# Kernel optimization log

Measured on AMD Instinct MI355X. Metric: run time of the kernel, lower is better.

## Reference

```python
import jax, jax.numpy as jnp
import numpy as np

H = 16      # num_heads
HD = 64     # head_dim
W = 1024    # local window size
G = 256     # number of global tokens
EPS = 1e-6
NEG = -1e30


def setup_inputs() -> dict:
    key = jax.random.key(0)
    ks = jax.random.split(key, 7)
    B, S, D = 1, 8192, 1024
    inner = H * HD
    s = 0.02
    return {
        "x": jax.random.normal(ks[0], (B, S, D), jnp.float32),
        "norm_w": jnp.ones((D,), jnp.float32),
        "w_q": jax.random.normal(ks[1], (D, inner), jnp.float32) * s,
        "w_k": jax.random.normal(ks[2], (D, inner), jnp.float32) * s,
        "w_v": jax.random.normal(ks[3], (D, inner), jnp.float32) * s,
        "w_out": jax.random.normal(ks[4], (inner, D), jnp.float32) * s,
        "scorer_w": jax.random.normal(ks[5], (D, 1), jnp.float32) * s,
        "scorer_b": jnp.zeros((1,), jnp.float32),
    }


def reference(x, norm_w, w_q, w_k, w_v, w_out, scorer_w, scorer_b):
    B, S, D = x.shape
    # pre-norm (RMSNorm)
    h = x * jax.lax.rsqrt(jnp.mean(x * x, axis=-1, keepdims=True) + EPS) * norm_w

    def proj(w):  # [B,S,D] -> [B,H,S,HD]
        return jnp.einsum('bsd,de->bse', h, w).reshape(B, S, H, HD).transpose(0, 2, 1, 3)

    q, k, v = proj(w_q), proj(w_k), proj(w_v)
    scale = HD ** -0.5

    # --- local block attention (non-overlapping causal windows) ---
    nW = S // W
    qw = q.reshape(B, H, nW, W, HD)
    kw = k.reshape(B, H, nW, W, HD)
    vw = v.reshape(B, H, nW, W, HD)
    ll = jnp.einsum('bhnqd,bhnkd->bhnqk', qw, kw) * scale  # [B,H,nW,W,W]
    cm = jnp.tril(jnp.ones((W, W), bool))
    ll = jnp.where(cm, ll, NEG).reshape(B, H, S, W)

    # --- sparse global attention over top-G important tokens ---
    scores = (jnp.einsum('bsd,do->bso', h, scorer_w) + scorer_b)[..., 0]  # [B,S]
    _, idx = jax.lax.top_k(scores, G)                                     # [B,G]
    kg = jnp.take_along_axis(k, idx[:, None, :, None], axis=2)            # [B,H,G,HD]
    vg = jnp.take_along_axis(v, idx[:, None, :, None], axis=2)
    lg = jnp.einsum('bhsd,bhgd->bhsg', q, kg) * scale                     # [B,H,S,G]
    pos = jnp.arange(S)
    gmask = idx[:, None, None, :] <= pos[None, None, :, None]             # causal: global pos <= query pos
    lg = jnp.where(gmask, lg, NEG)

    # --- joint softmax over local window + global tokens ---
    attn = jax.nn.softmax(jnp.concatenate([ll, lg], axis=-1), axis=-1)    # [B,H,S,W+G]
    a_loc = attn[..., :W].reshape(B, H, nW, W, W)
    o = jnp.einsum('bhnqk,bhnkd->bhnqd', a_loc, vw).reshape(B, H, S, HD)
    o = o + jnp.einsum('bhsg,bhgd->bhsd', attn[..., W:], vg)

    o = o.transpose(0, 2, 1, 3).reshape(B, S, H * HD)
    return x + jnp.einsum('bse,ed->bsd', o, w_out)  # residual
```

## Files before the change

kernel.cpp:

```cpp
#include <hip/hip_runtime.h>
#include <stdint.h>

#define S_LEN 8192
#define DIM   1024
#define NH    16
#define HD    64
#define WIN   1024
#define GTOK  256
#define QKV_STRIDE (3 * DIM)

typedef __attribute__((ext_vector_type(8))) short bf16x8;
typedef __attribute__((ext_vector_type(4))) float f32x4;
typedef __attribute__((ext_vector_type(16))) float f32x16;
typedef unsigned short u16;
typedef uint32_t u32;

__device__ __forceinline__ u16 f2bf(float f) {
  union { float f; uint32_t u; } v; v.f = f;
  uint32_t r = v.u + 0x7fffu + ((v.u >> 16) & 1u);
  return (u16)(r >> 16);
}
__device__ __forceinline__ float bf2f(u16 b) {
  union { uint32_t u; float f; } v; v.u = ((uint32_t)b) << 16;
  return v.f;
}
__device__ __forceinline__ uint32_t cvtpk(float a, float b) {
  uint32_t r;
  asm("v_cvt_pk_bf16_f32 %0, %1, %2" : "=v"(r) : "v"(a), "v"(b));
  return r;
}

__device__ __forceinline__ void gload_lds16(const void* g, void* l) {
  __builtin_amdgcn_global_load_lds((const __attribute__((address_space(1))) void*)g,
                                   (__attribute__((address_space(3))) void*)l, 16, 0, 0);
}

__global__ __launch_bounds__(256) void rmsnorm_score_kernel(
    const float* __restrict__ x, const float* __restrict__ nw,
    const float* __restrict__ sw, const float* __restrict__ sb,
    u16* __restrict__ h, float* __restrict__ scores, int* __restrict__ cnt) {
  int row = blockIdx.x, tid = threadIdx.x;
  const float4* xr = (const float4*)(x + (size_t)row * DIM);
  float4 v = xr[tid];
  float ss = v.x * v.x + v.y * v.y + v.z * v.z + v.w * v.w;
#pragma unroll
  for (int o = 32; o >= 1; o >>= 1) ss += __shfl_xor(ss, o);
  __shared__ float red[4], red2[4];
  int wv = tid >> 6;
  if ((tid & 63) == 0) red[wv] = ss;
  __syncthreads();
  ss = red[0] + red[1] + red[2] + red[3];
  float rn = rsqrtf(ss * (1.0f / DIM) + 1e-6f);
  float4 w4 = ((const float4*)nw)[tid];
  float h0 = v.x * rn * w4.x, h1 = v.y * rn * w4.y;
  float h2 = v.z * rn * w4.z, h3 = v.w * rn * w4.w;
  uint64_t pack = (uint64_t)f2bf(h0) | ((uint64_t)f2bf(h1) << 16) |
                  ((uint64_t)f2bf(h2) << 32) | ((uint64_t)f2bf(h3) << 48);
  *(uint64_t*)(h + (size_t)row * DIM + tid * 4) = pack;
  float4 s4 = ((const float4*)sw)[tid];
  float sc = h0 * s4.x + h1 * s4.y + h2 * s4.z + h3 * s4.w;
#pragma unroll
  for (int o = 32; o >= 1; o >>= 1) sc += __shfl_xor(sc, o);
  if ((tid & 63) == 0) red2[wv] = sc;
  __syncthreads();
  if (tid == 0) {
    scores[row] = red2[0] + red2[1] + red2[2] + red2[3] + sb[0];
    cnt[row] = 0;
  }
}

__global__ __launch_bounds__(256) void transpose_w_kernel(
    const float* __restrict__ wq, const float* __restrict__ wk,
    const float* __restrict__ wv, const float* __restrict__ wo,
    u16* __restrict__ wqkvT, u16* __restrict__ woutT) {
  __shared__ float tile[32][33];
  int z = blockIdx.z;
  const float* src = (z == 0) ? wq : (z == 1) ? wk : (z == 2) ? wv : wo;
  u16* dst = (z < 3) ? (wqkvT + (size_t)z * DIM * DIM) : woutT;
  int tx = threadIdx.x, ty = threadIdx.y;
  int n0 = blockIdx.x * 32, k0 = blockIdx.y * 32;
#pragma unroll
  for (int i = 0; i < 4; i++)
    tile[ty + i * 8][tx] = src[(size_t)(k0 + ty + i * 8) * DIM + n0 + tx];
  __syncthreads();
#pragma unroll
  for (int i = 0; i < 4; i++)
    dst[(size_t)(n0 + ty + i * 8) * DIM + k0 + tx] = f2bf(tile[tx][ty + i * 8]);
}

__global__ __launch_bounds__(256) void topk_count_kernel(
    const float* __restrict__ scores, int* __restrict__ cnt) {
  __shared__ float sj[1024];
  int jbase = blockIdx.y * 1024;
  for (int t = threadIdx.x; t < 1024; t += 256) sj[t] = scores[jbase + t];
  __syncthreads();
  int i = blockIdx.x * 256 + threadIdx.x;
  float my = scores[i];
  int c = 0;
  const float4* s4 = (const float4*)sj;
#pragma unroll 4
  for (int j = 0; j < 256; j++) {
    float4 v = s4[j];
    int b = jbase + j * 4;
    c += (v.x > my) || (v.x == my && (b + 0) < i);
    c += (v.y > my) || (v.y == my && (b + 1) < i);
    c += (v.z > my) || (v.z == my && (b + 2) < i);
    c += (v.w > my) || (v.w == my && (b + 3) < i);
  }
  if (c) atomicAdd(&cnt[i], c);
}

__global__ __launch_bounds__(256) void topk_scatter_kernel(
    const int* __restrict__ cnt, int* __restrict__ gidx) {
  int i = blockIdx.x * 256 + threadIdx.x;
  int c = cnt[i];
  if (c < GTOK) gidx[c] = i;
}

__global__ __launch_bounds__(128) void gather_kernel(
    const u16* __restrict__ qkv, const int* __restrict__ gidx,
    u16* __restrict__ kg, u16* __restrict__ vg) {
  int g = blockIdx.x, t = threadIdx.x;
  size_t src = (size_t)gidx[g] * QKV_STRIDE;
  *(bf16x8*)(kg + (size_t)g * DIM + t * 8) = *(const bf16x8*)(qkv + src + DIM + t * 8);
  *(bf16x8*)(vg + (size_t)g * DIM + t * 8) = *(const bf16x8*)(qkv + src + 2 * DIM + t * 8);
}

template <int RESID>
__global__ __launch_bounds__(512, 2) void gemm256_kernel(
    const u16* __restrict__ A, const u16* __restrict__ B,
    u16* __restrict__ Cb, float* __restrict__ Cf, const float* __restrict__ X,
    int M, int N, int K) {
  __shared__ __align__(16) u16 As[3][256 * 64];
  __shared__ __align__(16) u16 Bs[3][128 * 64];
  const int tid = threadIdx.x;
  const int wave = tid >> 6, lane = tid & 63;
  const int l15 = lane & 15, l4 = lane >> 4;
  const int wr = wave >> 1, wc = wave & 1;
  const int mbase = blockIdx.x * 256, nbase = blockIdx.y * 128;
  const int srow = lane >> 3, schunk = lane & 7;
  const int gcol = (schunk ^ srow) * 8;

  auto stage = [&](int tt, int b) {
    const int kt = tt << 6;
#pragma unroll
    for (int q = 0; q < 4; q++) {
      int row = wave * 32 + q * 8;
      gload_lds16(A + (size_t)(mbase + row + srow) * K + kt + gcol, &As[b][row * 64]);
    }
#pragma unroll
    for (int q = 0; q < 2; q++) {
      int row = wave * 16 + q * 8;
      gload_lds16(B + (size_t)(nbase + row + srow) * K + kt + gcol, &Bs[b][row * 64]);
    }
  };

  const int nt = K >> 6;
  f32x4 acc[4][4] = {};

  stage(0, 0);
  stage(1, 1);
  asm volatile("s_waitcnt vmcnt(6)" ::: "memory");
  __builtin_amdgcn_s_barrier();
  __builtin_amdgcn_sched_barrier(0);

  int cur = 0;
  for (int t = 0; t < nt; t++) {
    int pre = cur + 2; if (pre >= 3) pre -= 3;
    if (t + 2 < nt) stage(t + 2, pre);
    const u16* Ab = &As[cur][0];
    const u16* Bb = &Bs[cur][0];
    bf16x8 bfr[4][2], af[4][2];
#pragma unroll
    for (int nf = 0; nf < 4; nf++) {
      int row = wc * 64 + nf * 16 + l15;
#pragma unroll
      for (int kk = 0; kk < 2; kk++)
        bfr[nf][kk] = *(const bf16x8*)(Bb + row * 64 + (((kk * 4 + l4) ^ (l15 & 7)) * 8));
    }
#pragma unroll
    for (int mi = 0; mi < 4; mi++) {
      int row = wr * 64 + mi * 16 + l15;
#pragma unroll
      for (int kk = 0; kk < 2; kk++)
        af[mi][kk] = *(const bf16x8*)(Ab + row * 64 + (((kk * 4 + l4) ^ (l15 & 7)) * 8));
    }
    __builtin_amdgcn_s_setprio(1);
#pragma unroll
    for (int mi = 0; mi < 4; mi++)
#pragma unroll
      for (int nf = 0; nf < 4; nf++)
#pragma unroll
        for (int kk = 0; kk < 2; kk++)
          acc[mi][nf] = __builtin_amdgcn_mfma_f32_16x16x32_bf16(af[mi][kk], bfr[nf][kk],
                                                                acc[mi][nf], 0, 0, 0);
    __builtin_amdgcn_s_setprio(0);
    if (t + 1 < nt) {
      if (t + 2 < nt) asm volatile("s_waitcnt vmcnt(6)" ::: "memory");
      else            asm volatile("s_waitcnt vmcnt(0)" ::: "memory");
      __builtin_amdgcn_s_barrier();
      __builtin_amdgcn_sched_barrier(0);
    }
    cur = (cur + 1 == 3) ? 0 : cur + 1;
  }

#pragma unroll
  for (int mi = 0; mi < 4; mi++) {
#pragma unroll
    for (int nf = 0; nf < 4; nf++) {
#pragma unroll
      for (int r = 0; r < 4; r++) {
        int row = mbase + wr * 64 + mi * 16 + l4 * 4 + r;
        int col = nbase + wc * 64 + nf * 16 + l15;
        float v = acc[mi][nf][r];
        if (RESID) Cf[(size_t)row * N + col] = X[(size_t)row * N + col] + v;
        else       Cb[(size_t)row * N + col] = f2bf(v);
      }
    }
  }
}

__global__ __launch_bounds__(512) void attn_kernel(
    const u16* __restrict__ qkv, const u16* __restrict__ kg,
    const u16* __restrict__ vg, const int* __restrict__ gidx,
    u16* __restrict__ o) {
  __shared__ u16 kT[2][64][72];
  __shared__ u16 vT[2][64][72];
  __shared__ int gposLds[2][64];
  const int tid = threadIdx.x, wave = tid >> 6, lane = tid & 63;
  const int l31 = lane & 31, hi = lane >> 5;
  const int win = blockIdx.x >> 1, pair = blockIdx.x & 1;
  const int wbase = win * WIN;
  const int hoff = blockIdx.y * HD;

  const int skey = tid >> 3, sd8 = (tid & 7) * 8;
  const int vcol = skey ^ ((sd8 >> 4) << 4);

  bf16x8 nk, nv;
  int ng = 0;
  {
    const u16* base = qkv + (size_t)(wbase + skey) * QKV_STRIDE + hoff + sd8;
    nk = *(const bf16x8*)(base + DIM);
    nv = *(const bf16x8*)(base + 2 * DIM);
  }

  for (int sp = 0; sp < 2; sp++) {
    const int j = sp ? (3 - pair) : pair;
    const int qsbase = wbase + j * 256;
    const int nLocal = (j + 1) * 4;
    const int nTiles = nLocal + GTOK / 64;
    const int qrow = qsbase + wave * 32 + l31;
    const int qwmax = qsbase + wave * 32 + 31;

    bf16x8 qf[4];
    {
      const float SC2 = 0.125f * 1.44269504088896f;
      const u16* qptr = qkv + (size_t)qrow * QKV_STRIDE + hoff + hi * 8;
#pragma unroll
      for (int ks = 0; ks < 4; ks++) {
        bf16x8 raw = *(const bf16x8*)(qptr + ks * 16);
        bf16x8 sc;
#pragma unroll
        for (int jj = 0; jj < 8; jj++) sc[jj] = (short)f2bf(bf2f((u16)raw[jj]) * SC2);
        qf[ks] = sc;
      }
    }

    f32x16 acc0 = {}, acc1 = {};
    float mr = -3.0e38f, lr = 0.f;

    __syncthreads();

    for (int t = 0; t < nTiles; t++) {
      const int p = t & 1;
      const bool isLocal = (t < nLocal);
      const int tbase = wbase + t * 64;
      *(bf16x8*)(&kT[p][skey][sd8]) = nk;
#pragma unroll
      for (int jj = 0; jj < 8; jj++) vT[p][sd8 + jj][vcol] = (u16)nv[jj];
      if (!isLocal && tid < 64) gposLds[p][tid] = ng;
      {
        const int nt = t + 1;
        const u16 *ksrc = nullptr, *vsrc = nullptr;
        if (nt < nLocal) {
          const u16* base = qkv + (size_t)(wbase + nt * 64 + skey) * QKV_STRIDE + hoff + sd8;
          ksrc = base + DIM; vsrc = base + 2 * DIM;
        } else if (nt < nTiles) {
          size_t grow = (size_t)((nt - nLocal) * 64 + skey) * DIM + hoff + sd8;
          ksrc = kg + grow; vsrc = vg + grow;
          if (tid < 64) ng = gidx[(nt - nLocal) * 64 + tid];
        } else if (sp == 0) {
          const u16* base = qkv + (size_t)(wbase + skey) * QKV_STRIDE + hoff + sd8;
          ksrc = base + DIM; vsrc = base + 2 * DIM;
        }
        if (ksrc) { nk = *(const bf16x8*)(ksrc); nv = *(const bf16x8*)(vsrc); }
      }
      __syncthreads();

      if (isLocal && tbase > qwmax) continue;

      float sv[32];
      __builtin_amdgcn_s_setprio(1);
#pragma unroll
      for (int kb = 0; kb < 2; kb++) {
        const u16* krow = &kT[p][kb * 32 + l31][hi * 8];
        bf16x8 k0 = *(const bf16x8*)(krow);
        bf16x8 k1 = *(const bf16x8*)(krow + 16);
        bf16x8 k2 = *(const bf16x8*)(krow + 32);
        bf16x8 k3 = *(const bf16x8*)(krow + 48);
        f32x16 z = {};
        z = __builtin_amdgcn_mfma_f32_32x32x16_bf16(k0, qf[0], z, 0, 0, 0);
        z = __builtin_amdgcn_mfma_f32_32x32x16_bf16(k1, qf[1], z, 0, 0, 0);
        z = __builtin_amdgcn_mfma_f32_32x32x16_bf16(k2, qf[2], z, 0, 0, 0);
        z = __builtin_amdgcn_mfma_f32_32x32x16_bf16(k3, qf[3], z, 0, 0, 0);
#pragma unroll
        for (int r = 0; r < 16; r++) sv[kb * 16 + r] = z[r];
      }
      __builtin_amdgcn_s_setprio(0);

      if (isLocal) {
        const int lim = qrow - tbase;
        if (lim < 63) {
#pragma unroll
          for (int kb = 0; kb < 2; kb++)
#pragma unroll
            for (int r = 0; r < 16; r++) {
              int crow = kb * 32 + (r & 3) + 8 * (r >> 2) + 4 * hi;
              if (crow > lim) sv[kb * 16 + r] = -3.0e38f;
            }
        }
      } else {
#pragma unroll
        for (int kb = 0; kb < 2; kb++)
#pragma unroll
          for (int r = 0; r < 16; r++) {
            int kpos = gposLds[p][kb * 32 + (r & 3) + 8 * (r >> 2) + 4 * hi];
            if (kpos > qrow) sv[kb * 16 + r] = -3.0e38f;
          }
      }

      float m0 = sv[0], m1 = sv[1], m2 = sv[2], m3 = sv[3];
#pragma unroll
      for (int i = 4; i < 32; i += 4) {
        m0 = fmaxf(m0, sv[i]);     m1 = fmaxf(m1, sv[i + 1]);
        m2 = fmaxf(m2, sv[i + 2]); m3 = fmaxf(m3, sv[i + 3]);
      }
      float vmax = fmaxf(fmaxf(m0, m1), fmaxf(m2, m3));
      vmax = fmaxf(vmax, __shfl_xor(vmax, 32));
      if (__any(vmax > mr + 11.0f)) {
        float mn = fmaxf(mr, vmax);
        float al = exp2f(mr - mn);
        lr *= al;
        mr = mn;
#pragma unroll
        for (int i = 0; i < 16; i++) { acc0[i] *= al; acc1[i] *= al; }
      }
      float s0 = 0.f, s1 = 0.f, s2 = 0.f, s3 = 0.f;
#pragma unroll
      for (int i = 0; i < 32; i += 4) {
        float p0 = exp2f(sv[i] - mr),     p1 = exp2f(sv[i + 1] - mr);
        float p2 = exp2f(sv[i + 2] - mr), p3 = exp2f(sv[i + 3] - mr);
        sv[i] = p0; sv[i + 1] = p1; sv[i + 2] = p2; sv[i + 3] = p3;
        s0 += p0; s1 += p1; s2 += p2; s3 += p3;
      }
      float ps = (s0 + s1) + (s2 + s3);
      ps += __shfl_xor(ps, 32);
      lr += ps;

      bf16x8 pf[4];
#pragma unroll
      for (int q4 = 0; q4 < 4; q4++) {
        int b = q4 * 8;
        uint32_t w0 = cvtpk(sv[b + 0], sv[b + 1]);
        uint32_t w1 = cvtpk(sv[b + 2], sv[b + 3]);
        uint32_t w2 = cvtpk(sv[b + 4], sv[b + 5]);
        uint32_t w3 = cvtpk(sv[b + 6], sv[b + 7]);
        uint32_t w0s = __shfl_xor((int)w0, 32), w2s = __shfl_xor((int)w2, 32);
        uint32_t w1s = __shfl_xor((int)w1, 32), w3s = __shfl_xor((int)w3, 32);
        union { uint32_t w[4]; bf16x8 v; } u;
        u.w[0] = hi ? w2s : w0;
        u.w[1] = hi ? w3s : w1;
        u.w[2] = hi ? w2 : w0s;
        u.w[3] = hi ? w3 : w1s;
        pf[q4] = u.v;
      }

      __builtin_amdgcn_s_setprio(1);
#pragma unroll
      for (int dblk = 0; dblk < 2; dblk++) {
        const int swz = (dblk * 2 + (l31 >> 4)) << 4;
        const u16* vrow = &vT[p][dblk * 32 + l31][0];
        f32x16 a = dblk ? acc1 : acc0;
#pragma unroll
        for (int ksg = 0; ksg < 4; ksg++) {
          bf16x8 vf = *(const bf16x8*)(vrow + ((ksg * 16 + hi * 8) ^ swz));
          a = __builtin_amdgcn_mfma_f32_32x32x16_bf16(vf, pf[ksg], a, 0, 0, 0);
        }
        if (dblk) acc1 = a; else acc0 = a;
      }
      __builtin_amdgcn_s_setprio(0);
    }

    float inv = 1.0f / lr;
#pragma unroll
    for (int dblk = 0; dblk < 2; dblk++) {
      f32x16 a = dblk ? acc1 : acc0;
#pragma unroll
      for (int g = 0; g < 4; g++) {
        uint64_t pk = (uint64_t)f2bf(a[g * 4 + 0] * inv)
                    | ((uint64_t)f2bf(a[g * 4 + 1] * inv) << 16)
                    | ((uint64_t)f2bf(a[g * 4 + 2] * inv) << 32)
                    | ((uint64_t)f2bf(a[g * 4 + 3] * inv) << 48);
        *(uint64_t*)(o + (size_t)qrow * DIM + hoff + dblk * 32 + g * 8 + 4 * hi) = pk;
      }
    }
  }
}

extern "C" void kernel_launch(void* const* d_in, const int* in_sizes, int n_in,
                              void* d_out, int out_size, void* d_ws, size_t ws_size,
                              hipStream_t stream) {
  const float* x  = (const float*)d_in[0];
  const float* nw = (const float*)d_in[1];
  const float* wq = (const float*)d_in[2];
  const float* wk = (const float*)d_in[3];
  const float* wv = (const float*)d_in[4];
  const float* wo = (const float*)d_in[5];
  const float* sw = (const float*)d_in[6];
  const float* sb = (const float*)d_in[7];
  float* out = (float*)d_out;

  char* ws = (char*)d_ws;
  size_t off = 0;
  auto alloc = [&](size_t b) {
    char* p = ws + off;
    off = (off + b + 255) & ~(size_t)255;
    return p;
  };
  u16*   h      = (u16*)alloc((size_t)S_LEN * DIM * 2);
  u16*   wqkvT  = (u16*)alloc((size_t)3 * DIM * DIM * 2);
  u16*   woutT  = (u16*)alloc((size_t)DIM * DIM * 2);
  u16*   qkv    = (u16*)alloc((size_t)S_LEN * 3 * DIM * 2);
  u16*   obuf   = (u16*)alloc((size_t)S_LEN * DIM * 2);
  float* scores = (float*)alloc((size_t)S_LEN * 4);
  int*   cnt    = (int*)alloc((size_t)S_LEN * 4);
  int*   gidx   = (int*)alloc((size_t)GTOK * 4);
  u16*   kgbuf  = (u16*)alloc((size_t)GTOK * DIM * 2);
  u16*   vgbuf  = (u16*)alloc((size_t)GTOK * DIM * 2);

  transpose_w_kernel<<<dim3(32, 32, 4), dim3(32, 8), 0, stream>>>(wq, wk, wv, wo, wqkvT, woutT);
  rmsnorm_score_kernel<<<dim3(S_LEN), dim3(256), 0, stream>>>(x, nw, sw, sb, h, scores, cnt);
  topk_count_kernel<<<dim3(32, 8), dim3(256), 0, stream>>>(scores, cnt);
  topk_scatter_kernel<<<dim3(S_LEN / 256), dim3(256), 0, stream>>>(cnt, gidx);
  gemm256_kernel<0><<<dim3(32, 24), dim3(512), 0, stream>>>(h, wqkvT, qkv, nullptr, nullptr,
                                                            S_LEN, 3 * DIM, DIM);
  gather_kernel<<<dim3(GTOK), dim3(128), 0, stream>>>(qkv, gidx, kgbuf, vgbuf);
  attn_kernel<<<dim3(16, NH), dim3(512), 0, stream>>>(qkv, kgbuf, vgbuf, gidx, obuf);
  gemm256_kernel<1><<<dim3(32, 8), dim3(512), 0, stream>>>(obuf, woutT, nullptr, out, x,
                                                           S_LEN, DIM, DIM);
}
```

Measured before the change: 219.8 us.

## Process both query strips in a single pass over shared K/V tiles

The attention block used to handle its two 256-row query strips one after the other, reloading local and global K/V tiles for each. Now it loads both strips' queries up front and streams the K/V tiles once (sized for the longer strip), running online softmax for each strip against every staged tile. This removes the repeated tile loads, the extra LDS staging and barriers, and the global K/V reread. In exchange each thread holds twice the query fragments, accumulators and softmax state, which raises register pressure and may lower occupancy or cause spills at 512 threads.

After: 219.2 us. About the same (-0.3%).

```diff
diff --git a/kernel.cpp b/kernel.cpp
--- a/kernel.cpp
+++ b/kernel.cpp
@@ -233,8 +233,35 @@
   const int wbase = win * WIN;
   const int hoff = blockIdx.y * HD;
 
+  const int jA = pair, jB = 3 - pair;
+  const int qsA = wbase + jA * 256, qsB = wbase + jB * 256;
+  const int nLocB = (jB + 1) * 4;
+  const int nTiles = nLocB + GTOK / 64;
+  const int qrowA = qsA + wave * 32 + l31, qwmaxA = qsA + wave * 32 + 31;
+  const int qrowB = qsB + wave * 32 + l31, qwmaxB = qsB + wave * 32 + 31;
+
   const int skey = tid >> 3, sd8 = (tid & 7) * 8;
   const int vcol = skey ^ ((sd8 >> 4) << 4);
+
+  bf16x8 qfA[4], qfB[4];
+  {
+    const float SC2 = 0.125f * 1.44269504088896f;
+    const u16* qpA = qkv + (size_t)qrowA * QKV_STRIDE + hoff + hi * 8;
+    const u16* qpB = qkv + (size_t)qrowB * QKV_STRIDE + hoff + hi * 8;
+#pragma unroll
+    for (int ks = 0; ks < 4; ks++) {
+      bf16x8 ra = *(const bf16x8*)(qpA + ks * 16);
+      bf16x8 rb = *(const bf16x8*)(qpB + ks * 16);
+      bf16x8 sa, sb2;
+#pragma unroll
+      for (int jj = 0; jj < 8; jj++) {
+        sa[jj]  = (short)f2bf(bf2f((u16)ra[jj]) * SC2);
+        sb2[jj] = (short)f2bf(bf2f((u16)rb[jj]) * SC2);
+      }
+      qfA[ks] = sa;
+      qfB[ks] = sb2;
+    }
+  }
 
   bf16x8 nk, nv;
   int ng = 0;
@@ -244,175 +271,160 @@
     nv = *(const bf16x8*)(base + 2 * DIM);
   }
 
-  for (int sp = 0; sp < 2; sp++) {
-    const int j = sp ? (3 - pair) : pair;
-    const int qsbase = wbase + j * 256;
-    const int nLocal = (j + 1) * 4;
-    const int nTiles = nLocal + GTOK / 64;
-    const int qrow = qsbase + wave * 32 + l31;
-    const int qwmax = qsbase + wave * 32 + 31;
-
-    bf16x8 qf[4];
-    {
-      const float SC2 = 0.125f * 1.44269504088896f;
-      const u16* qptr = qkv + (size_t)qrow * QKV_STRIDE + hoff + hi * 8;
-#pragma unroll
-      for (int ks = 0; ks < 4; ks++) {
-        bf16x8 raw = *(const bf16x8*)(qptr + ks * 16);
-        bf16x8 sc;
-#pragma unroll
-        for (int jj = 0; jj < 8; jj++) sc[jj] = (short)f2bf(bf2f((u16)raw[jj]) * SC2);
-        qf[ks] = sc;
-      }
-    }
-
-    f32x16 acc0 = {}, acc1 = {};
-    float mr = -3.0e38f, lr = 0.f;
-
-    __syncthreads();
-
-    for (int t = 0; t < nTiles; t++) {
-      const int p = t & 1;
-      const bool isLocal = (t < nLocal);
-      const int tbase = wbase + t * 64;
-      *(bf16x8*)(&kT[p][skey][sd8]) = nk;
-#pragma unroll
-      for (int jj = 0; jj < 8; jj++) vT[p][sd8 + jj][vcol] = (u16)nv[jj];
-      if (!isLocal && tid < 64) gposLds[p][tid] = ng;
-      {
-        const int nt = t + 1;
-        const u16 *ksrc = nullptr, *vsrc = nullptr;
-        if (nt < nLocal) {
-          const u16* base = qkv + (size_t)(wbase + nt * 64 + skey) * QKV_STRIDE + hoff + sd8;
-          ksrc = base + DIM; vsrc = base + 2 * DIM;
-        } else if (nt < nTiles) {
-          size_t grow = (size_t)((nt - nLocal) * 64 + skey) * DIM + hoff + sd8;
-          ksrc = kg + grow; vsrc = vg + grow;
-          if (tid < 64) ng = gidx[(nt - nLocal) * 64 + tid];
-        } else if (sp == 0) {
-          const u16* base = qkv + (size_t)(wbase + skey) * QKV_STRIDE + hoff + sd8;
-          ksrc = base + DIM; vsrc = base + 2 * DIM;
-        }
-        if (ksrc) { nk = *(const bf16x8*)(ksrc); nv = *(const bf16x8*)(vsrc); }
-      }
-      __syncthreads();
-
-      if (isLocal && tbase > qwmax) continue;
-
-      float sv[32];
-      __builtin_amdgcn_s_setprio(1);
-#pragma unroll
-      for (int kb = 0; kb < 2; kb++) {
-        const u16* krow = &kT[p][kb * 32 + l31][hi * 8];
-        bf16x8 k0 = *(const bf16x8*)(krow);
-        bf16x8 k1 = *(const bf16x8*)(krow + 16);
-        bf16x8 k2 = *(const bf16x8*)(krow + 32);
-        bf16x8 k3 = *(const bf16x8*)(krow + 48);
-        f32x16 z = {};
-        z = __builtin_amdgcn_mfma_f32_32x32x16_bf16(k0, qf[0], z, 0, 0, 0);
-        z = __builtin_amdgcn_mfma_f32_32x32x16_bf16(k1, qf[1], z, 0, 0, 0);
-        z = __builtin_amdgcn_mfma_f32_32x32x16_bf16(k2, qf[2], z, 0, 0, 0);
-        z = __builtin_amdgcn_mfma_f32_32x32x16_bf16(k3, qf[3], z, 0, 0, 0);
-#pragma unroll
-        for (int r = 0; r < 16; r++) sv[kb * 16 + r] = z[r];
-      }
-      __builtin_amdgcn_s_setprio(0);
-
-      if (isLocal) {
-        const int lim = qrow - tbase;
-        if (lim < 63) {
-#pragma unroll
-          for (int kb = 0; kb < 2; kb++)
-#pragma unroll
-            for (int r = 0; r < 16; r++) {
-              int crow = kb * 32 + (r & 3) + 8 * (r >> 2) + 4 * hi;
-              if (crow > lim) sv[kb * 16 + r] = -3.0e38f;
-            }
-        }
-      } else {
+  f32x16 accA0 = {}, accA1 = {}, accB0 = {}, accB1 = {};
+  float mrA = -3.0e38f, lrA = 0.f, mrB = -3.0e38f, lrB = 0.f;
+
+  auto computeStream = [&](const bf16x8* qf, f32x16& a0, f32x16& a1,
+                           float& mr, float& lr, int qrow,
+                           bool isLocal, int tbase, int p) {
+    float sv[32];
+    __builtin_amdgcn_s_setprio(1);
+#pragma unroll
+    for (int kb = 0; kb < 2; kb++) {
+      const u16* krow = &kT[p][kb * 32 + l31][hi * 8];
+      bf16x8 k0 = *(const bf16x8*)(krow);
+      bf16x8 k1 = *(const bf16x8*)(krow + 16);
+      bf16x8 k2 = *(const bf16x8*)(krow + 32);
+      bf16x8 k3 = *(const bf16x8*)(krow + 48);
+      f32x16 z = {};
+      z = __builtin_amdgcn_mfma_f32_32x32x16_bf16(k0, qf[0], z, 0, 0, 0);
+      z = __builtin_amdgcn_mfma_f32_32x32x16_bf16(k1, qf[1], z, 0, 0, 0);
+      z = __builtin_amdgcn_mfma_f32_32x32x16_bf16(k2, qf[2], z, 0, 0, 0);
+      z = __builtin_amdgcn_mfma_f32_32x32x16_bf16(k3, qf[3], z, 0, 0, 0);
+#pragma unroll
+      for (int r = 0; r < 16; r++) sv[kb * 16 + r] = z[r];
+    }
+    __builtin_amdgcn_s_setprio(0);
+
+    if (isLocal) {
+      const int lim = qrow - tbase;
+      if (lim < 63) {
 #pragma unroll
         for (int kb = 0; kb < 2; kb++)
 #pragma unroll
           for (int r = 0; r < 16; r++) {
-            int kpos = gposLds[p][kb * 32 + (r & 3) + 8 * (r >> 2) + 4 * hi];
-            if (kpos > qrow) sv[kb * 16 + r] = -3.0e38f;
+            int crow = kb * 32 + (r & 3) + 8 * (r >> 2) + 4 * hi;
+            if (crow > lim) sv[kb * 16 + r] = -3.0e38f;
           }
       }
-
-      float m0 = sv[0], m1 = sv[1], m2 = sv[2], m3 = sv[3];
-#pragma unroll
-      for (int i = 4; i < 32; i += 4) {
-        m0 = fmaxf(m0, sv[i]);     m1 = fmaxf(m1, sv[i + 1]);
-        m2 = fmaxf(m2, sv[i + 2]); m3 = fmaxf(m3, sv[i + 3]);
+    } else {
+#pragma unroll
+      for (int kb = 0; kb < 2; kb++)
+#pragma unroll
+        for (int r = 0; r < 16; r++) {
+          int kpos = gposLds[p][kb * 32 + (r & 3) + 8 * (r >> 2) + 4 * hi];
+          if (kpos > qrow) sv[kb * 16 + r] = -3.0e38f;
+        }
+    }
+
+    float m0 = sv[0], m1 = sv[1], m2 = sv[2], m3 = sv[3];
+#pragma unroll
+    for (int i = 4; i < 32; i += 4) {
+      m0 = fmaxf(m0, sv[i]);     m1 = fmaxf(m1, sv[i + 1]);
+      m2 = fmaxf(m2, sv[i + 2]); m3 = fmaxf(m3, sv[i + 3]);
+    }
+    float vmax = fmaxf(fmaxf(m0, m1), fmaxf(m2, m3));
+    vmax = fmaxf(vmax, __shfl_xor(vmax, 32));
+    if (__any(vmax > mr + 11.0f)) {
+      float mn = fmaxf(mr, vmax);
+      float al = exp2f(mr - mn);
+      lr *= al;
+      mr = mn;
+#pragma unroll
+      for (int i = 0; i < 16; i++) { a0[i] *= al; a1[i] *= al; }
+    }
+    float s0 = 0.f, s1 = 0.f, s2 = 0.f, s3 = 0.f;
+#pragma unroll
+    for (int i = 0; i < 32; i += 4) {
+      float p0 = exp2f(sv[i] - mr),     p1 = exp2f(sv[i + 1] - mr);
+      float p2 = exp2f(sv[i + 2] - mr), p3 = exp2f(sv[i + 3] - mr);
+      sv[i] = p0; sv[i + 1] = p1; sv[i + 2] = p2; sv[i + 3] = p3;
+      s0 += p0; s1 += p1; s2 += p2; s3 += p3;
+    }
+    float ps = (s0 + s1) + (s2 + s3);
+    ps += __shfl_xor(ps, 32);
+    lr += ps;
+
+    bf16x8 pf[4];
+#pragma unroll
+    for (int q4 = 0; q4 < 4; q4++) {
+      int b = q4 * 8;
+      uint32_t w0 = cvtpk(sv[b + 0], sv[b + 1]);
+      uint32_t w1 = cvtpk(sv[b + 2], sv[b + 3]);
+      uint32_t w2 = cvtpk(sv[b + 4], sv[b + 5]);
+      uint32_t w3 = cvtpk(sv[b + 6], sv[b + 7]);
+      uint32_t w0s = __shfl_xor((int)w0, 32), w2s = __shfl_xor((int)w2, 32);
+      uint32_t w1s = __shfl_xor((int)w1, 32), w3s = __shfl_xor((int)w3, 32);
+      union { uint32_t w[4]; bf16x8 v; } u;
+      u.w[0] = hi ? w2s : w0;
+      u.w[1] = hi ? w3s : w1;
+      u.w[2] = hi ? w2 : w0s;
+      u.w[3] = hi ? w3 : w1s;
+      pf[q4] = u.v;
+    }
+
+    __builtin_amdgcn_s_setprio(1);
+#pragma unroll
+    for (int dblk = 0; dblk < 2; dblk++) {
+      const int swz = (dblk * 2 + (l31 >> 4)) << 4;
+      const u16* vrow = &vT[p][dblk * 32 + l31][0];
+      f32x16 a = dblk ? a1 : a0;
+#pragma unroll
+      for (int ksg = 0; ksg < 4; ksg++) {
+        bf16x8 vf = *(const bf16x8*)(vrow + ((ksg * 16 + hi * 8) ^ swz));
+        a = __builtin_amdgcn_mfma_f32_32x32x16_bf16(vf, pf[ksg], a, 0, 0, 0);
       }
-      float vmax = fmaxf(fmaxf(m0, m1), fmaxf(m2, m3));
-      vmax = fmaxf(vmax, __shfl_xor(vmax, 32));
-      if (__any(vmax > mr + 11.0f)) {
-        float mn = fmaxf(mr, vmax);
-        float al = exp2f(mr - mn);
-        lr *= al;
-        mr = mn;
-#pragma unroll
-        for (int i = 0; i < 16; i++) { acc0[i] *= al; acc1[i] *= al; }
+      if (dblk) a1 = a; else a0 = a;
+    }
+    __builtin_amdgcn_s_setprio(0);
+  };
+
+  for (int t = 0; t < nTiles; t++) {
+    const int p = t & 1;
+    const bool isLocal = (t < nLocB);
+    const int tbase = wbase + t * 64;
+    *(bf16x8*)(&kT[p][skey][sd8]) = nk;
+#pragma unroll
+    for (int jj = 0; jj < 8; jj++) vT[p][sd8 + jj][vcol] = (u16)nv[jj];
+    if (!isLocal && tid < 64) gposLds[p][tid] = ng;
+    {
+      const int nt = t + 1;
+      const u16 *ksrc = nullptr, *vsrc = nullptr;
+      if (nt < nLocB) {
+        const u16* base = qkv + (size_t)(wbase + nt * 64 + skey) * QKV_STRIDE + hoff + sd8;
+        ksrc = base + DIM; vsrc = base + 2 * DIM;
+      } else if (nt < nTiles) {
+        size_t grow = (size_t)((nt - nLocB) * 64 + skey) * DIM + hoff + sd8;
+        ksrc = kg + grow; vsrc = vg + grow;
+        if (tid < 64) ng = gidx[(nt - nLocB) * 64 + tid];
       }
-      float s0 = 0.f, s1 = 0.f, s2 = 0.f, s3 = 0.f;
-#pragma unroll
-      for (int i = 0; i < 32; i += 4) {
-        float p0 = exp2f(sv[i] - mr),     p1 = exp2f(sv[i + 1] - mr);
-        float p2 = exp2f(sv[i + 2] - mr), p3 = exp2f(sv[i + 3] - mr);
-        sv[i] = p0; sv[i + 1] = p1; sv[i + 2] = p2; sv[i + 3] = p3;
-        s0 += p0; s1 += p1; s2 += p2; s3 += p3;
-      }
-      float ps = (s0 + s1) + (s2 + s3);
-      ps += __shfl_xor(ps, 32);
-      lr += ps;
-
-      bf16x8 pf[4];
-#pragma unroll
-      for (int q4 = 0; q4 < 4; q4++) {
-        int b = q4 * 8;
-        uint32_t w0 = cvtpk(sv[b + 0], sv[b + 1]);
-        uint32_t w1 = cvtpk(sv[b + 2], sv[b + 3]);
-        uint32_t w2 = cvtpk(sv[b + 4], sv[b + 5]);
-        uint32_t w3 = cvtpk(sv[b + 6], sv[b + 7]);
-        uint32_t w0s = __shfl_xor((int)w0, 32), w2s = __shfl_xor((int)w2, 32);
-        uint32_t w1s = __shfl_xor((int)w1, 32), w3s = __shfl_xor((int)w3, 32);
-        union { uint32_t w[4]; bf16x8 v; } u;
-        u.w[0] = hi ? w2s : w0;
-        u.w[1] = hi ? w3s : w1;
-        u.w[2] = hi ? w2 : w0s;
-        u.w[3] = hi ? w3 : w1s;
-        pf[q4] = u.v;
-      }
-
-      __builtin_amdgcn_s_setprio(1);
-#pragma unroll
-      for (int dblk = 0; dblk < 2; dblk++) {
-        const int swz = (dblk * 2 + (l31 >> 4)) << 4;
-        const u16* vrow = &vT[p][dblk * 32 + l31][0];
-        f32x16 a = dblk ? acc1 : acc0;
-#pragma unroll
-        for (int ksg = 0; ksg < 4; ksg++) {
-          bf16x8 vf = *(const bf16x8*)(vrow + ((ksg * 16 + hi * 8) ^ swz));
-          a = __builtin_amdgcn_mfma_f32_32x32x16_bf16(vf, pf[ksg], a, 0, 0, 0);
-        }
-        if (dblk) acc1 = a; else acc0 = a;
-      }
-      __builtin_amdgcn_s_setprio(0);
-    }
-
-    float inv = 1.0f / lr;
-#pragma unroll
-    for (int dblk = 0; dblk < 2; dblk++) {
-      f32x16 a = dblk ? acc1 : acc0;
-#pragma unroll
-      for (int g = 0; g < 4; g++) {
-        uint64_t pk = (uint64_t)f2bf(a[g * 4 + 0] * inv)
-                    | ((uint64_t)f2bf(a[g * 4 + 1] * inv) << 16)
-                    | ((uint64_t)f2bf(a[g * 4 + 2] * inv) << 32)
-                    | ((uint64_t)f2bf(a[g * 4 + 3] * inv) << 48);
-        *(uint64_t*)(o + (size_t)qrow * DIM + hoff + dblk * 32 + g * 8 + 4 * hi) = pk;
-      }
+      if (ksrc) { nk = *(const bf16x8*)(ksrc); nv = *(const bf16x8*)(vsrc); }
+    }
+    __syncthreads();
+
+    if (!(isLocal && tbase > qwmaxA))
+      computeStream(qfA, accA0, accA1, mrA, lrA, qrowA, isLocal, tbase, p);
+    if (!(isLocal && tbase > qwmaxB))
+      computeStream(qfB, accB0, accB1, mrB, lrB, qrowB, isLocal, tbase, p);
+  }
+
+  float invA = 1.0f / lrA, invB = 1.0f / lrB;
+#pragma unroll
+  for (int dblk = 0; dblk < 2; dblk++) {
+    f32x16 a = dblk ? accA1 : accA0;
+    f32x16 b = dblk ? accB1 : accB0;
+#pragma unroll
+    for (int g = 0; g < 4; g++) {
+      uint64_t pkA = (uint64_t)f2bf(a[g * 4 + 0] * invA)
+                   | ((uint64_t)f2bf(a[g * 4 + 1] * invA) << 16)
+                   | ((uint64_t)f2bf(a[g * 4 + 2] * invA) << 32)
+                   | ((uint64_t)f2bf(a[g * 4 + 3] * invA) << 48);
+      *(uint64_t*)(o + (size_t)qrowA * DIM + hoff + dblk * 32 + g * 8 + 4 * hi) = pkA;
+      uint64_t pkB = (uint64_t)f2bf(b[g * 4 + 0] * invB)
+                   | ((uint64_t)f2bf(b[g * 4 + 1] * invB) << 16)
+                   | ((uint64_t)f2bf(b[g * 4 + 2] * invB) << 32)
+                   | ((uint64_t)f2bf(b[g * 4 + 3] * invB) << 48);
+      *(uint64_t*)(o + (size_t)qrowB * DIM + hoff + dblk * 32 + g * 8 + 4 * hi) = pkB;
     }
   }
 }
```
